# Performance work log

Hardware: AMD Instinct MI355X
Metric: run time of the kernel (lower is better)

## Reference

```python
import jax, jax.numpy as jnp
import numpy as np

EPS = 1e-07
MO, DO = 8, 16  # output caps maps/dims
NUM_ITERS = 2

def squash(s, axis=-1):
    sq = jnp.sum(s * s, axis=axis)                     # squared norm
    safe = jnp.sqrt(sq + EPS)
    factor = sq / (1.0 + sq)
    unit = s / safe[..., None]
    return factor[..., None] * unit


def setup_inputs() -> dict:
    key = jax.random.key(0)
    k1, k2, k3 = jax.random.split(key, 3)
    B, MI, H, W, DI = 8, 8, 64, 64, 16
    x = jax.random.normal(k1, (B, MI, H, W, DI), dtype=jnp.float32)
    conv_w = jax.random.normal(k2, (MO * DO, MI * DI, 3, 3), dtype=jnp.float32) * 0.05
    conv_b = jax.random.normal(k3, (MO * DO,), dtype=jnp.float32) * 0.05
    b_logits = jnp.zeros((1, MO, H, W, MI), dtype=jnp.float32)  # routing logits self.b
    return {"x": x, "conv_w": conv_w, "conv_b": conv_b, "b_logits": b_logits}


def reference(x, conv_w, conv_b, b_logits):
    B, MI, H, W, DI = x.shape
    # [B, MI, H, W, DI] -> [B, MI*DI, H, W]
    x2 = jnp.transpose(x, (0, 1, 4, 2, 3)).reshape(B, MI * DI, H, W)
    y = jax.lax.conv_general_dilated(
        x2, conv_w, window_strides=(1, 1), padding=((1, 1), (1, 1)),
        dimension_numbers=("NCHW", "OIHW", "NCHW"))
    y = y + conv_b[None, :, None, None]
    hn, wn = y.shape[2], y.shape[3]
    # view [B, MO, DO, h, w, -1] then permute -> [B, MO, h, w, 1, DO]
    pred = jnp.transpose(y.reshape(B, MO, DO, hn, wn, -1), (0, 1, 3, 4, 5, 2))

    # --- dynamic routing (faithful to Agreement_Routing_Down.forward) ---
    c = jax.nn.softmax(b_logits, axis=-1)              # [1, MO, h, w, MI]
    out = squash(jnp.sum(c[..., None] * pred, axis=-2))  # [B, MO, h, w, DO]
    b_batch = b_logits
    for _ in range(NUM_ITERS):
        b_batch = b_batch + jnp.sum(pred * out[..., None, :], axis=-1)
        c = jax.nn.softmax(b_batch, axis=-1)
        out = squash(jnp.sum(pred * c[..., None], axis=-2))
    return out
```

## Files before the change

### kernel.cpp

```cpp
#include <hip/hip_runtime.h>

#define EPSF 1e-7f

typedef _Float16 f16x8 __attribute__((ext_vector_type(8)));
typedef float f32x4 __attribute__((ext_vector_type(4)));

#define LDS_A_BYTES 67584
#define LDS_B_BYTES 32768
#define LDS_TOTAL (LDS_A_BYTES + 2 * LDS_B_BYTES)

__global__ void repack_kernel(const float* __restrict__ cw, _Float16* __restrict__ wTh) {
    int e = blockIdx.x * 256 + threadIdx.x;
    if (e >= 9 * 16 * 128 * 8) return;
    int sub = e & 7;
    int co  = (e >> 3) & 127;
    int g   = (e >> 10) & 15;
    int t   = e >> 14;
    wTh[e] = (_Float16)cw[(co * 128 + (g * 8 + sub)) * 9 + t];
}

__global__ __launch_bounds__(256, 1) void conv_mfma_kernel(
    const float* __restrict__ x,
    const _Float16* __restrict__ wTh,
    const float* __restrict__ bias,
    float* __restrict__ out)
{
    extern __shared__ char smem[];
    char* A = smem;
    char* Bb[2] = { smem + LDS_A_BYTES, smem + LDS_A_BYTES + LDS_B_BYTES };

    const int tid  = (int)threadIdx.x;
    const int lane = tid & 63;
    const int w_id = tid >> 6;
    const int q    = lane >> 4;
    const int m15  = lane & 15;
    const int blk  = (int)blockIdx.x;
    const int b    = blk >> 5;
    const int h0   = (blk & 31) << 1;

    f16x8 breg[8];
#pragma unroll
    for (int it = 0; it < 8; ++it)
        breg[it] = *(const f16x8*)(wTh + (tid + it * 256) * 8);

    for (int i = 0; i < 17; ++i) {
        const int gi = tid + i * 256;
        if (gi < 4224) {
            const int g  = gi & 15;
            const int rw = gi >> 4;
            const int r  = rw / 66;
            const int wp = rw - r * 66;
            const int mi = g >> 1, di0 = (g & 1) << 3;
            const int gh = h0 - 1 + r, gw = wp - 1;
            f16x8 v = {0, 0, 0, 0, 0, 0, 0, 0};
            if ((unsigned)gh < 64u && (unsigned)gw < 64u) {
                const float* xp = x + ((((b * 8 + mi) * 64 + gh) * 64 + gw) * 16 + di0);
                const float4 lo = *(const float4*)xp;
                const float4 hi = *(const float4*)(xp + 4);
                v[0] = (_Float16)lo.x; v[1] = (_Float16)lo.y;
                v[2] = (_Float16)lo.z; v[3] = (_Float16)lo.w;
                v[4] = (_Float16)hi.x; v[5] = (_Float16)hi.y;
                v[6] = (_Float16)hi.z; v[7] = (_Float16)hi.w;
            }
            *(f16x8*)(A + r * 16896 + g * 1056 + wp * 16) = v;
        }
    }

#pragma unroll
    for (int it = 0; it < 8; ++it)
        *(f16x8*)(Bb[0] + (tid + it * 256) * 16) = breg[it];

    __syncthreads();

    const int wave_m = w_id >> 1, wave_n = w_id & 1;
    const char* aptr = A + wave_m * 16896 + q * 1056 + m15 * 16;

    f32x4 acc[4][4];
#pragma unroll
    for (int fn = 0; fn < 4; ++fn) {
        const float bv = bias[wave_n * 64 + fn * 16 + m15];
#pragma unroll
        for (int fm = 0; fm < 4; ++fm) {
            acc[fm][fn][0] = bv; acc[fm][fn][1] = bv;
            acc[fm][fn][2] = bv; acc[fm][fn][3] = bv;
        }
    }

#pragma unroll
    for (int kh = 0; kh < 3; ++kh) {
#pragma unroll
        for (int kw = 0; kw < 3; ++kw) {
            const int t = kh * 3 + kw;
            if (t < 8) {
#pragma unroll
                for (int it = 0; it < 8; ++it)
                    breg[it] = *(const f16x8*)(wTh + (t + 1) * 16384 + (tid + it * 256) * 8);
            }
            const char* bptr = Bb[t & 1] + q * 2048 + wave_n * 1024 + m15 * 16;
            const char* ap   = aptr + kh * 16896 + kw * 16;
#pragma unroll
            for (int kc = 0; kc < 4; ++kc) {
                f16x8 bf[4], af[4];
#pragma unroll
                for (int fn = 0; fn < 4; ++fn)
                    bf[fn] = *(const f16x8*)(bptr + kc * 8192 + fn * 256);
#pragma unroll
                for (int fm = 0; fm < 4; ++fm)
                    af[fm] = *(const f16x8*)(ap + kc * 4224 + fm * 256);
#pragma unroll
                for (int fm = 0; fm < 4; ++fm)
#pragma unroll
                    for (int fn = 0; fn < 4; ++fn)
                        acc[fm][fn] = __builtin_amdgcn_mfma_f32_16x16x32_f16(
                            af[fm], bf[fn], acc[fm][fn], 0, 0, 0);
            }
            if (t < 8) {
                char* wb = Bb[(t + 1) & 1];
#pragma unroll
                for (int it = 0; it < 8; ++it)
                    *(f16x8*)(wb + (tid + it * 256) * 16) = breg[it];
            }
            __syncthreads();
        }
    }

    char* Y = smem + w_id * 17408;
#pragma unroll
    for (int fm = 0; fm < 4; ++fm)
#pragma unroll
        for (int fn = 0; fn < 4; ++fn)
#pragma unroll
            for (int rg = 0; rg < 4; ++rg) {
                const int m = fm * 16 + q * 4 + rg;
                const int c = fn * 16 + m15;
                *(float*)(Y + m * 272 + c * 4) = acc[fm][fn][rg];
            }
    __syncthreads();

    const int h = h0 + wave_m;
#pragma unroll
    for (int i = 0; i < 4; ++i) {
        const int m   = i * 16 + m15;
        const int mol = q;
        const float* yp = (const float*)(Y + m * 272 + mol * 64);
        float4 v0 = *(const float4*)(yp);
        float4 v1 = *(const float4*)(yp + 4);
        float4 v2 = *(const float4*)(yp + 8);
        float4 v3 = *(const float4*)(yp + 12);
        float s = 0.f;
        s = fmaf(v0.x, v0.x, s); s = fmaf(v0.y, v0.y, s);
        s = fmaf(v0.z, v0.z, s); s = fmaf(v0.w, v0.w, s);
        s = fmaf(v1.x, v1.x, s); s = fmaf(v1.y, v1.y, s);
        s = fmaf(v1.z, v1.z, s); s = fmaf(v1.w, v1.w, s);
        s = fmaf(v2.x, v2.x, s); s = fmaf(v2.y, v2.y, s);
        s = fmaf(v2.z, v2.z, s); s = fmaf(v2.w, v2.w, s);
        s = fmaf(v3.x, v3.x, s); s = fmaf(v3.y, v3.y, s);
        s = fmaf(v3.z, v3.z, s); s = fmaf(v3.w, v3.w, s);
        const float mult = s / ((1.0f + s) * sqrtf(s + EPSF));
        v0.x *= mult; v0.y *= mult; v0.z *= mult; v0.w *= mult;
        v1.x *= mult; v1.y *= mult; v1.z *= mult; v1.w *= mult;
        v2.x *= mult; v2.y *= mult; v2.z *= mult; v2.w *= mult;
        v3.x *= mult; v3.y *= mult; v3.z *= mult; v3.w *= mult;
        const int mo = wave_n * 4 + mol;
        float* op = out + ((((b * 8 + mo) * 64 + h) * 64 + m) * 16);
        *(float4*)(op)      = v0;
        *(float4*)(op + 4)  = v1;
        *(float4*)(op + 8)  = v2;
        *(float4*)(op + 12) = v3;
    }
}

extern "C" void kernel_launch(void* const* d_in, const int* in_sizes, int n_in,
                              void* d_out, int out_size, void* d_ws, size_t ws_size,
                              hipStream_t stream) {
    const float* x  = (const float*)d_in[0];
    const float* cw = (const float*)d_in[1];
    const float* cb = (const float*)d_in[2];
    float* outp    = (float*)d_out;
    _Float16* wTh  = (_Float16*)d_ws;

    hipFuncSetAttribute((const void*)conv_mfma_kernel,
                        hipFuncAttributeMaxDynamicSharedMemorySize, LDS_TOTAL);
    hipLaunchKernelGGL(repack_kernel, dim3(576), dim3(256), 0, stream, cw, wTh);
    hipLaunchKernelGGL(conv_mfma_kernel, dim3(256), dim3(256), LDS_TOTAL, stream,
                       x, wTh, cb, outp);
}
```

Measured before the change: 94.98 us.

## Load conv weights directly from global, drop LDS weight buffers, use 512 threads

The conv kernel no longer stages weight taps in double-buffered LDS. Each wave now reads its B fragments straight from the repacked global weight buffer, which is L2-resident. The block grows to 8 waves with each wave covering half as many output rows, and LDS shrinks to just the input tile, so two blocks can fit per CU and the per-tap __syncthreads are removed. In exchange, every wave re-reads the weights from global/L2 with no prefetch. The Y scratch region is also resized so it still fits in the smaller LDS.

```diff
diff --git a/kernel.cpp b/kernel.cpp
--- a/kernel.cpp
+++ b/kernel.cpp
@@ -6,8 +6,7 @@
 typedef float f32x4 __attribute__((ext_vector_type(4)));
 
 #define LDS_A_BYTES 67584
-#define LDS_B_BYTES 32768
-#define LDS_TOTAL (LDS_A_BYTES + 2 * LDS_B_BYTES)
+#define LDS_TOTAL   69632
 
 __global__ void repack_kernel(const float* __restrict__ cw, _Float16* __restrict__ wTh) {
     int e = blockIdx.x * 256 + threadIdx.x;
@@ -19,7 +18,7 @@
     wTh[e] = (_Float16)cw[(co * 128 + (g * 8 + sub)) * 9 + t];
 }
 
-__global__ __launch_bounds__(256, 1) void conv_mfma_kernel(
+__global__ __launch_bounds__(512, 2) void conv_mfma_kernel(
     const float* __restrict__ x,
     const _Float16* __restrict__ wTh,
     const float* __restrict__ bias,
@@ -27,24 +26,20 @@
 {
     extern __shared__ char smem[];
     char* A = smem;
-    char* Bb[2] = { smem + LDS_A_BYTES, smem + LDS_A_BYTES + LDS_B_BYTES };
 
     const int tid  = (int)threadIdx.x;
     const int lane = tid & 63;
     const int w_id = tid >> 6;
     const int q    = lane >> 4;
     const int m15  = lane & 15;
+    const int wm   = w_id >> 1;
+    const int wn   = w_id & 1;
     const int blk  = (int)blockIdx.x;
     const int b    = blk >> 5;
     const int h0   = (blk & 31) << 1;
 
-    f16x8 breg[8];
-#pragma unroll
-    for (int it = 0; it < 8; ++it)
-        breg[it] = *(const f16x8*)(wTh + (tid + it * 256) * 8);
-
-    for (int i = 0; i < 17; ++i) {
-        const int gi = tid + i * 256;
+    for (int i = 0; i < 9; ++i) {
+        const int gi = tid + i * 512;
         if (gi < 4224) {
             const int g  = gi & 15;
             const int rw = gi >> 4;
@@ -65,68 +60,54 @@
             *(f16x8*)(A + r * 16896 + g * 1056 + wp * 16) = v;
         }
     }
-
-#pragma unroll
-    for (int it = 0; it < 8; ++it)
-        *(f16x8*)(Bb[0] + (tid + it * 256) * 16) = breg[it];
-
     __syncthreads();
 
-    const int wave_m = w_id >> 1, wave_n = w_id & 1;
-    const char* aptr = A + wave_m * 16896 + q * 1056 + m15 * 16;
-
-    f32x4 acc[4][4];
+    f32x4 acc[2][4];
 #pragma unroll
     for (int fn = 0; fn < 4; ++fn) {
-        const float bv = bias[wave_n * 64 + fn * 16 + m15];
+        const float bv = bias[wn * 64 + fn * 16 + m15];
 #pragma unroll
-        for (int fm = 0; fm < 4; ++fm) {
+        for (int fm = 0; fm < 2; ++fm) {
             acc[fm][fn][0] = bv; acc[fm][fn][1] = bv;
             acc[fm][fn][2] = bv; acc[fm][fn][3] = bv;
         }
     }
+
+    const char* aw = A + (wm >> 1) * 16896 + ((wm & 1) * 32 + m15) * 16;
 
 #pragma unroll
     for (int kh = 0; kh < 3; ++kh) {
 #pragma unroll
         for (int kw = 0; kw < 3; ++kw) {
             const int t = kh * 3 + kw;
-            if (t < 8) {
+            f16x8 bf[4][4];
 #pragma unroll
-                for (int it = 0; it < 8; ++it)
-                    breg[it] = *(const f16x8*)(wTh + (t + 1) * 16384 + (tid + it * 256) * 8);
-            }
-            const char* bptr = Bb[t & 1] + q * 2048 + wave_n * 1024 + m15 * 16;
-            const char* ap   = aptr + kh * 16896 + kw * 16;
+            for (int kc = 0; kc < 4; ++kc)
+#pragma unroll
+                for (int fn = 0; fn < 4; ++fn)
+                    bf[kc][fn] = *(const f16x8*)(wTh +
+                        ((size_t)((t * 16 + kc * 4 + q) * 128 + wn * 64 + fn * 16 + m15)) * 8);
 #pragma unroll
             for (int kc = 0; kc < 4; ++kc) {
-                f16x8 bf[4], af[4];
+                f16x8 af[2];
 #pragma unroll
-                for (int fn = 0; fn < 4; ++fn)
-                    bf[fn] = *(const f16x8*)(bptr + kc * 8192 + fn * 256);
+                for (int fm = 0; fm < 2; ++fm)
+                    af[fm] = *(const f16x8*)(aw + kh * 16896 + (kc * 4 + q) * 1056
+                                                + (fm * 16 + kw) * 16);
 #pragma unroll
-                for (int fm = 0; fm < 4; ++fm)
-                    af[fm] = *(const f16x8*)(ap + kc * 4224 + fm * 256);
-#pragma unroll
-                for (int fm = 0; fm < 4; ++fm)
+                for (int fm = 0; fm < 2; ++fm)
 #pragma unroll
                     for (int fn = 0; fn < 4; ++fn)
                         acc[fm][fn] = __builtin_amdgcn_mfma_f32_16x16x32_f16(
-                            af[fm], bf[fn], acc[fm][fn], 0, 0, 0);
+                            af[fm], bf[kc][fn], acc[fm][fn], 0, 0, 0);
             }
-            if (t < 8) {
-                char* wb = Bb[(t + 1) & 1];
-#pragma unroll
-                for (int it = 0; it < 8; ++it)
-                    *(f16x8*)(wb + (tid + it * 256) * 16) = breg[it];
-            }
-            __syncthreads();
         }
     }
 
-    char* Y = smem + w_id * 17408;
+    __syncthreads();
+    char* Y = smem + w_id * 8704;
 #pragma unroll
-    for (int fm = 0; fm < 4; ++fm)
+    for (int fm = 0; fm < 2; ++fm)
 #pragma unroll
         for (int fn = 0; fn < 4; ++fn)
 #pragma unroll
@@ -137,10 +118,11 @@
             }
     __syncthreads();
 
-    const int h = h0 + wave_m;
+    const int h  = h0 + (wm >> 1);
+    const int wb = (wm & 1) * 32;
 #pragma unroll
-    for (int i = 0; i < 4; ++i) {
-        const int m   = i * 16 + m15;
+    for (int it = 0; it < 2; ++it) {
+        const int m   = it * 16 + m15;
         const int mol = q;
         const float* yp = (const float*)(Y + m * 272 + mol * 64);
         float4 v0 = *(const float4*)(yp);
@@ -161,8 +143,8 @@
         v1.x *= mult; v1.y *= mult; v1.z *= mult; v1.w *= mult;
         v2.x *= mult; v2.y *= mult; v2.z *= mult; v2.w *= mult;
         v3.x *= mult; v3.y *= mult; v3.z *= mult; v3.w *= mult;
-        const int mo = wave_n * 4 + mol;
-        float* op = out + ((((b * 8 + mo) * 64 + h) * 64 + m) * 16);
+        const int mo = wn * 4 + mol;
+        float* op = out + ((((b * 8 + mo) * 64 + h) * 64 + (wb + m)) * 16);
         *(float4*)(op)      = v0;
         *(float4*)(op + 4)  = v1;
         *(float4*)(op + 8)  = v2;
@@ -182,6 +164,6 @@
     hipFuncSetAttribute((const void*)conv_mfma_kernel,
                         hipFuncAttributeMaxDynamicSharedMemorySize, LDS_TOTAL);
     hipLaunchKernelGGL(repack_kernel, dim3(576), dim3(256), 0, stream, cw, wTh);
-    hipLaunchKernelGGL(conv_mfma_kernel, dim3(256), dim3(256), LDS_TOTAL, stream,
+    hipLaunchKernelGGL(conv_mfma_kernel, dim3(256), dim3(512), LDS_TOTAL, stream,
                        x, wTh, cb, outp);
 }
```

Result: no change. 94.27 us (-0.7%).
